# Optimization experiments

Measured on AMD Instinct MI355X. Metric: run time of the kernel, lower is better.

Reference implementation:

```python
import jax, jax.numpy as jnp
import numpy as np

K = 40  # neighbors, self.k = 40 in the module
BN_EPS = 1e-5


def knn(x, k):
    # x: (B, C, N) -> indices of k nearest points (largest negative sq-dist)
    xx = jnp.sum(x * x, axis=1, keepdims=True)            # (B, 1, N)
    inner = -2.0 * jnp.einsum('bcn,bcm->bnm', x, x)       # (B, N, N)
    pd = -xx - inner - jnp.swapaxes(xx, 1, 2)             # (B, N, N) = -||xi-xj||^2
    _, idx = jax.lax.top_k(pd, k)                         # (B, N, k)
    return idx


def graph_cov(x, k):
    # Faithful port of get_graph_dynamic_covariance (dim9=False, idx=None)
    B, C, N = x.shape
    idx = knn(x, k)                                       # (B, N, k)
    xt = jnp.swapaxes(x, 1, 2)                            # (B, N, C)
    feature = xt[jnp.arange(B)[:, None, None], idx]       # gather: (B, N, k, C)
    xc = xt[:, :, None, :]                                # (B, N, 1, C)
    rel = feature - xc                                    # relative positions
    var = jnp.var(rel, axis=2, ddof=1)                    # torch.var is unbiased
    relf = rel * (1.0 - var)[:, :, None, :]
    relf = jnp.concatenate([jnp.broadcast_to(xc, rel.shape), relf], axis=3)
    norm = rel - jnp.mean(rel, axis=0)                    # mean over BATCH dim, as in source
    cov = jnp.einsum('bnkc,bnjc->bnkj', rel, norm)        # (B, N, k, k)
    out = jnp.concatenate([relf, cov], axis=3)            # (B, N, k, 2C+k)
    return jnp.transpose(out, (0, 3, 1, 2))               # (B, 2C+k, N, k)


def bn(x, g, b):
    # train-mode BatchNorm (batch statistics, biased variance), eps=1e-5
    axes = (0,) + tuple(range(2, x.ndim))
    m = jnp.mean(x, axis=axes, keepdims=True)
    v = jnp.var(x, axis=axes, keepdims=True)
    shp = (1, -1) + (1,) * (x.ndim - 2)
    return g.reshape(shp) * (x - m) * jax.lax.rsqrt(v + BN_EPS) + b.reshape(shp)


def blk(x, W, g, b):
    # Conv(1x1, no bias) + BN + LeakyReLU(0.2)
    return jax.nn.leaky_relu(bn(jnp.einsum('oi,bi...->bo...', W, x), g, b), 0.2)


def forward(x, l, W3, W4, W5, W6, W7, W8, W9, W10, W11, W12,
            g3, b3, g4, b4, g5, b5, g6, b6, g7, b7, g8, b8, g9, b9,
            g10, b10, g11, b11):
    B, _, N = x.shape
    rc = blk(blk(graph_cov(x, K), W3, g3, b3), W4, g4, b4)       # (B,64,N,K)
    rc_ = jnp.max(rc, axis=-1)                                    # (B,64,N)
    drc = blk(blk(graph_cov(rc_, K), W5, g5, b5), W6, g6, b6)
    drc_ = jnp.max(drc, axis=-1)                                  # (B,64,N)
    allf = jnp.concatenate([rc_, drc_], axis=1)                   # (B,128,N)
    h = jnp.max(blk(allf, W7, g7, b7), axis=-1, keepdims=True)    # (B,1024,1)
    lv = blk(l.reshape(B, -1, 1), W8, g8, b8)                     # (B,64,1)
    h = jnp.concatenate([h, lv], axis=1)                          # (B,1088,1)
    h = jnp.broadcast_to(h, (B, h.shape[1], N))
    h = jnp.concatenate([h, rc_, drc_], axis=1)                   # (B,1216,N)
    h = blk(h, W9, g9, b9)
    h = blk(h, W10, g10, b10)                                     # dropout is eval-mode identity
    h = blk(h, W11, g11, b11)
    return jnp.einsum('oi,bin->bon', W12, h)                      # (B,50,N)


def setup_inputs():
    key = jax.random.key(0)
    ks = jax.random.split(key, 12)
    B, N = 4, 2048
    d = {}
    d['x'] = jax.random.normal(ks[0], (B, 3, N), jnp.float32)
    lab = jax.random.randint(ks[1], (B,), 0, 16)
    d['l'] = jax.nn.one_hot(lab, 16, dtype=jnp.float32)
    wdims = {'W3': (64, 46), 'W4': (64, 64), 'W5': (64, 168), 'W6': (64, 64),
             'W7': (1024, 128), 'W8': (64, 16), 'W9': (512, 1216),
             'W10': (256, 512), 'W11': (128, 256), 'W12': (50, 128)}
    for i, (name, shp) in enumerate(wdims.items()):
        d[name] = jax.random.normal(ks[2 + i], shp, jnp.float32) / np.float32(np.sqrt(shp[1]))
    for name, c in [('g3', 64), ('g4', 64), ('g5', 64), ('g6', 64), ('g7', 1024),
                    ('g8', 64), ('g9', 512), ('g10', 256), ('g11', 128)]:
        d[name] = jnp.ones((c,), jnp.float32)
        d['b' + name[1:]] = jnp.zeros((c,), jnp.float32)
    return d


def reference(x, l, W3, W4, W5, W6, W7, W8, W9, W10, W11, W12,
              g3, b3, g4, b4, g5, b5, g6, b6, g7, b7, g8, b8, g9, b9,
              g10, b10, g11, b11):
    return forward(x, l, W3, W4, W5, W6, W7, W8, W9, W10, W11, W12,
                   g3, b3, g4, b4, g5, b5, g6, b6, g7, b7, g8, b8, g9, b9,
                   g10, b10, g11, b11)
```

## Files before the change

### kernel.cpp

```cpp
#include <hip/hip_runtime.h>
#include <math.h>

#define NB 4
#define NP 2048
#define KNN 40
#define BEPS 1e-5f
#define NSLOT 64
#define CMCH 16

typedef unsigned long long u64;

static __device__ __forceinline__ float leaky(float x) { return x >= 0.f ? x : 0.2f * x; }

static __device__ __forceinline__ u64 keyOf(float v, int m) {
  unsigned u = __float_as_uint(v);
  u ^= (u >> 31) ? 0xFFFFFFFFu : 0x80000000u;
  return ((u64)u << 32) | (unsigned)(NP - 1 - m);
}
static __device__ __forceinline__ u64 umax64(u64 a, u64 b) { return a > b ? a : b; }

__global__ __launch_bounds__(256) void canary_kernel(float* __restrict__ out, int n, float val) {
  int i = blockIdx.x*256 + threadIdx.x;
  if (i < n) out[i] = val;
}

__global__ __launch_bounds__(256) void knn3_kernel(const float* __restrict__ x, int* __restrict__ idx) {
  int b = blockIdx.y, n = blockIdx.x, tid = threadIdx.x;
  __shared__ float pd[NP];
  __shared__ u64 red[256];
  __shared__ u64 red2[32];
  __shared__ int sh_w;
  float xn0 = x[(b*3+0)*NP+n], xn1 = x[(b*3+1)*NP+n], xn2 = x[(b*3+2)*NP+n];
  float xxn = __fadd_rn(__fadd_rn(__fmul_rn(xn0,xn0), __fmul_rn(xn1,xn1)), __fmul_rn(xn2,xn2));
  for (int m = tid; m < NP; m += 256) {
    float m0 = x[(b*3+0)*NP+m], m1 = x[(b*3+1)*NP+m], m2 = x[(b*3+2)*NP+m];
    float xxm = __fadd_rn(__fadd_rn(__fmul_rn(m0,m0), __fmul_rn(m1,m1)), __fmul_rn(m2,m2));
    float dot = __fmaf_rn(xn2, m2, __fmaf_rn(xn1, m1, __fmul_rn(xn0, m0)));
    float inner = __fmul_rn(-2.f, dot);
    pd[m] = __fsub_rn(__fsub_rn(-xxm, inner), xxn);
  }
  __syncthreads();
  u64 myBest = 0;
  #pragma unroll
  for (int j = 0; j < 8; ++j) myBest = umax64(myBest, keyOf(pd[tid + j*256], tid + j*256));
  for (int kk = 0; kk < KNN; ++kk) {
    red[tid] = myBest;
    __syncthreads();
    if (tid < 32) {
      u64 h = red[tid];
      #pragma unroll
      for (int j = 1; j < 8; ++j) h = umax64(h, red[tid + j*32]);
      red2[tid] = h;
    }
    __syncthreads();
    if (tid == 0) {
      u64 h = red2[0];
      #pragma unroll
      for (int j = 1; j < 32; ++j) h = umax64(h, red2[j]);
      int w = NP - 1 - (int)(h & 0xFFFFFFFFu);
      idx[(b*NP+n)*KNN + kk] = w;
      pd[w] = -INFINITY;
      sh_w = w;
    }
    __syncthreads();
    if ((sh_w & 255) == tid) {
      u64 nb = 0;
      #pragma unroll
      for (int j = 0; j < 8; ++j) nb = umax64(nb, keyOf(pd[tid + j*256], tid + j*256));
      myBest = nb;
    }
  }
}

__global__ __launch_bounds__(256) void xx64_kernel(const float* __restrict__ rc, float* __restrict__ xx) {
  int i = blockIdx.x*256 + threadIdx.x;
  if (i >= NB*NP) return;
  const float* p = &rc[(size_t)i*64];
  float s = __fmul_rn(p[0], p[0]);
  #pragma unroll
  for (int c = 1; c < 64; ++c) s = __fadd_rn(s, __fmul_rn(p[c], p[c]));
  xx[i] = s;
}

__global__ __launch_bounds__(256) void knn64_kernel(const float* __restrict__ rc, const float* __restrict__ xx,
                                                    int* __restrict__ idx) {
  int b = blockIdx.y, n0 = blockIdx.x*2, tid = threadIdx.x;
  __shared__ float pd[2][NP];
  __shared__ float xn[2][64];
  __shared__ u64 red[256];
  __shared__ u64 red2[32];
  __shared__ int sh_w;
  if (tid < 128) xn[tid >> 6][tid & 63] = rc[((size_t)b*NP + n0 + (tid >> 6))*64 + (tid & 63)];
  __syncthreads();
  float xxn0 = xx[b*NP + n0], xxn1 = xx[b*NP + n0 + 1];
  for (int m = tid; m < NP; m += 256) {
    const float* xm = &rc[((size_t)b*NP + m)*64];
    float v0 = xm[0];
    float d0 = __fmul_rn(xn[0][0], v0);
    float d1 = __fmul_rn(xn[1][0], v0);
    #pragma unroll
    for (int c = 1; c < 64; ++c) {
      float v = xm[c];
      d0 = __fmaf_rn(xn[0][c], v, d0);
      d1 = __fmaf_rn(xn[1][c], v, d1);
    }
    float xxm = xx[b*NP + m];
    pd[0][m] = __fsub_rn(__fsub_rn(-xxm, __fmul_rn(-2.f, d0)), xxn0);
    pd[1][m] = __fsub_rn(__fsub_rn(-xxm, __fmul_rn(-2.f, d1)), xxn1);
  }
  __syncthreads();
  for (int q = 0; q < 2; ++q) {
    u64 myBest = 0;
    #pragma unroll
    for (int j = 0; j < 8; ++j) myBest = umax64(myBest, keyOf(pd[q][tid + j*256], tid + j*256));
    for (int kk = 0; kk < KNN; ++kk) {
      red[tid] = myBest;
      __syncthreads();
      if (tid < 32) {
        u64 h = red[tid];
        #pragma unroll
        for (int j = 1; j < 8; ++j) h = umax64(h, red[tid + j*32]);
        red2[tid] = h;
      }
      __syncthreads();
      if (tid == 0) {
        u64 h = red2[0];
        #pragma unroll
        for (int j = 1; j < 32; ++j) h = umax64(h, red2[j]);
        int w = NP - 1 - (int)(h & 0xFFFFFFFFu);
        idx[((size_t)b*NP + n0 + q)*KNN + kk] = w;
        pd[q][w] = -INFINITY;
        sh_w = w;
      }
      __syncthreads();
      if ((sh_w & 255) == tid) {
        u64 nb = 0;
        #pragma unroll
        for (int j = 0; j < 8; ++j) nb = umax64(nb, keyOf(pd[q][tid + j*256], tid + j*256));
        myBest = nb;
      }
    }
    __syncthreads();
  }
}


__global__ __launch_bounds__(256) void s1a_kernel(
    const float* __restrict__ x, const int* __restrict__ idx1, const float* __restrict__ W3,
    double* __restrict__ stslots, float* __restrict__ y)
{
  int b = blockIdx.y, n = blockIdx.x, tid = threadIdx.x;
  __shared__ int sidx[4][KNN];
  __shared__ float rs[KNN][4];
  __shared__ float ns[KNN][4];
  __shared__ float scale[3];
  __shared__ __align__(16) float feat[KNN*48];
  __shared__ float w3s[64*48];
  __shared__ double sred[4][64];

  for (int i = tid; i < 4*KNN; i += 256) sidx[i/KNN][i%KNN] = idx1[((i/KNN)*NP + n)*KNN + (i%KNN)];
  for (int i = tid; i < 64*48; i += 256) { int o = i/48, ci = i%48; w3s[i] = (ci < 46) ? W3[o*46+ci] : 0.f; }
  __syncthreads();
  for (int i = tid; i < KNN*3; i += 256) {
    int k = i/3, c = i%3;
    float ctr = x[(b*3+c)*NP + n];
    float r = x[(b*3+c)*NP + sidx[b][k]] - ctr;
    float s = 0.f;
    for (int b2 = 0; b2 < 4; ++b2) s += x[(b2*3+c)*NP + sidx[b2][k]] - x[(b2*3+c)*NP + n];
    rs[k][c] = r; ns[k][c] = r - 0.25f*s;
  }
  __syncthreads();
  if (tid < 3) {
    float s = 0.f; for (int k = 0; k < KNN; ++k) s += rs[k][tid];
    float m = s/(float)KNN; float v = 0.f;
    for (int k = 0; k < KNN; ++k) { float d = rs[k][tid]-m; v += d*d; }
    scale[tid] = 1.f - v/(float)(KNN-1);
  }
  __syncthreads();
  for (int i = tid; i < KNN*48; i += 256) {
    int k = i/48, ci = i%48; float v;
    if (ci < 3) v = x[(b*3+ci)*NP+n];
    else if (ci < 6) v = rs[k][ci-3]*scale[ci-3];
    else if (ci < 46) { int j = ci-6; v = rs[k][0]*ns[j][0] + rs[k][1]*ns[j][1] + rs[k][2]*ns[j][2]; }
    else v = 0.f;
    feat[i] = v;
  }
  __syncthreads();

  int o = tid & 63, kg = tid >> 6;
  float acc[10];
  #pragma unroll
  for (int t = 0; t < 10; ++t) acc[t] = 0.f;
  for (int ci4 = 0; ci4 < 12; ++ci4) {
    float w0 = w3s[o*48+ci4*4+0], w1 = w3s[o*48+ci4*4+1], w2 = w3s[o*48+ci4*4+2], w3c = w3s[o*48+ci4*4+3];
    #pragma unroll
    for (int t = 0; t < 10; ++t) {
      float4 f4 = *(const float4*)&feat[(kg*10+t)*48 + ci4*4];
      acc[t] += f4.x*w0 + f4.y*w1 + f4.z*w2 + f4.w*w3c;
    }
  }
  size_t bn40 = (size_t)(b*NP+n)*KNN;
  #pragma unroll
  for (int t = 0; t < 10; ++t) y[(bn40 + kg*10+t)*64 + o] = acc[t];
  double s = 0.0, s2 = 0.0;
  #pragma unroll
  for (int t = 0; t < 10; ++t) { double a = acc[t]; s += a; s2 += a*a; }
  int slot = (blockIdx.y*NP + blockIdx.x) & (NSLOT-1);
  sred[kg][o] = s; __syncthreads();
  if (kg == 0) atomicAdd(&stslots[slot*128 + o], sred[0][o]+sred[1][o]+sred[2][o]+sred[3][o]);
  __syncthreads();
  sred[kg][o] = s2; __syncthreads();
  if (kg == 0) atomicAdd(&stslots[slot*128 + 64 + o], sred[0][o]+sred[1][o]+sred[2][o]+sred[3][o]);
}

__global__ __launch_bounds__(256) void s2a_kernel(
    const float* __restrict__ rc, const int* __restrict__ idx2, const float* __restrict__ W5,
    double* __restrict__ stslots, float* __restrict__ y)
{
  int b = blockIdx.y, n = blockIdx.x, tid = threadIdx.x;
  __shared__ int sidx[4][KNN];
  __shared__ float rsT[64*41];
  __shared__ float nsT[64*41];
  __shared__ float scale[64];
  __shared__ __align__(16) float feat[KNN*168];
  __shared__ double sred[4][64];

  for (int i = tid; i < 4*KNN; i += 256) sidx[i/KNN][i%KNN] = idx2[((i/KNN)*NP + n)*KNN + (i%KNN)];
  __syncthreads();
  for (int i = tid; i < KNN*64; i += 256) {
    int k = i >> 6, c = i & 63;
    float ctr = rc[((size_t)(b*NP+n))*64 + c];
    float r = rc[((size_t)(b*NP) + sidx[b][k])*64 + c] - ctr;
    float s = 0.f;
    for (int b2 = 0; b2 < 4; ++b2)
      s += rc[((size_t)(b2*NP) + sidx[b2][k])*64 + c] - rc[((size_t)(b2*NP+n))*64 + c];
    rsT[c*41+k] = r; nsT[c*41+k] = r - 0.25f*s;
  }
  __syncthreads();
  if (tid < 64) {
    int c = tid;
    float s = 0.f; for (int k = 0; k < KNN; ++k) s += rsT[c*41+k];
    float m = s/(float)KNN; float v = 0.f;
    for (int k = 0; k < KNN; ++k) { float d = rsT[c*41+k]-m; v += d*d; }
    scale[c] = 1.f - v/(float)(KNN-1);
  }
  __syncthreads();
  for (int i = tid; i < KNN*128; i += 256) {
    int k = i >> 7, ci = i & 127;
    float v;
    if (ci < 64) v = rc[((size_t)(b*NP+n))*64 + ci];
    else v = rsT[(ci-64)*41 + k]*scale[ci-64];
    feat[k*168 + ci] = v;
  }
  for (int p = tid; p < KNN*KNN; p += 256) {
    int k = p/KNN, j = p%KNN;
    float acc = __fmul_rn(rsT[k], nsT[j]);
    #pragma unroll 8
    for (int c = 1; c < 64; ++c) acc = __fmaf_rn(rsT[c*41+k], nsT[c*41+j], acc);
    feat[k*168 + 128 + j] = acc;
  }
  __syncthreads();

  int o = tid & 63, kg = tid >> 6;
  float acc[10];
  #pragma unroll
  for (int t = 0; t < 10; ++t) acc[t] = 0.f;
  for (int ci4 = 0; ci4 < 42; ++ci4) {
    float4 wv = *(const float4*)&W5[(size_t)o*168 + ci4*4];
    #pragma unroll
    for (int t = 0; t < 10; ++t) {
      float4 f4 = *(const float4*)&feat[(kg*10+t)*168 + ci4*4];
      acc[t] += f4.x*wv.x + f4.y*wv.y + f4.z*wv.z + f4.w*wv.w;
    }
  }
  size_t bn40 = (size_t)(b*NP+n)*KNN;
  #pragma unroll
  for (int t = 0; t < 10; ++t) y[(bn40 + kg*10+t)*64 + o] = acc[t];
  double s = 0.0, s2 = 0.0;
  #pragma unroll
  for (int t = 0; t < 10; ++t) { double a = acc[t]; s += a; s2 += a*a; }
  int slot = (blockIdx.y*NP + blockIdx.x) & (NSLOT-1);
  sred[kg][o] = s; __syncthreads();
  if (kg == 0) atomicAdd(&stslots[slot*128 + o], sred[0][o]+sred[1][o]+sred[2][o]+sred[3][o]);
  __syncthreads();
  sred[kg][o] = s2; __syncthreads();
  if (kg == 0) atomicAdd(&stslots[slot*128 + 64 + o], sred[0][o]+sred[1][o]+sred[2][o]+sred[3][o]);
}

__global__ __launch_bounds__(256) void mid_kernel(
    float* __restrict__ y, const float* __restrict__ W,
    const double* __restrict__ stp, const float* __restrict__ gv, const float* __restrict__ bv,
    double* __restrict__ stslots)
{
  int b = blockIdx.y, n = blockIdx.x, tid = threadIdx.x;
  __shared__ float m_s[64], sc_s[64], bo_s[64];
  __shared__ __align__(16) float ytile[KNN*68];
  __shared__ double sred[4][64];
  const double INV_M1 = 1.0/327680.0;

  if (tid < 64) {
    double md = stp[tid]*INV_M1;
    double vd = stp[64+tid]*INV_M1 - md*md;
    m_s[tid] = (float)md;
    sc_s[tid] = gv[tid]/sqrtf((float)vd + BEPS);
    bo_s[tid] = bv[tid];
  }
  __syncthreads();
  size_t bn40 = (size_t)(b*NP+n)*KNN;
  for (int i = tid; i < KNN*64; i += 256) {
    int k = i >> 6, c = i & 63;
    float v = y[(bn40 + k)*64 + c];
    ytile[k*68+c] = leaky(sc_s[c]*(v - m_s[c]) + bo_s[c]);
  }
  __syncthreads();
  int o = tid & 63, kg = tid >> 6;
  float acc2[10];
  #pragma unroll
  for (int t = 0; t < 10; ++t) acc2[t] = 0.f;
  for (int c4 = 0; c4 < 16; ++c4) {
    float4 wv = *(const float4*)&W[(size_t)o*64 + c4*4];
    #pragma unroll
    for (int t = 0; t < 10; ++t) {
      float4 y4 = *(const float4*)&ytile[(kg*10+t)*68 + c4*4];
      acc2[t] += y4.x*wv.x + y4.y*wv.y + y4.z*wv.z + y4.w*wv.w;
    }
  }
  #pragma unroll
  for (int t = 0; t < 10; ++t) y[(bn40 + kg*10+t)*64 + o] = acc2[t];
  double s = 0.0, s2 = 0.0;
  #pragma unroll
  for (int t = 0; t < 10; ++t) { double a = acc2[t]; s += a; s2 += a*a; }
  int slot = (blockIdx.y*NP + blockIdx.x) & (NSLOT-1);
  sred[kg][o] = s; __syncthreads();
  if (kg == 0) atomicAdd(&stslots[slot*128 + o], sred[0][o]+sred[1][o]+sred[2][o]+sred[3][o]);
  __syncthreads();
  sred[kg][o] = s2; __syncthreads();
  if (kg == 0) atomicAdd(&stslots[slot*128 + 64 + o], sred[0][o]+sred[1][o]+sred[2][o]+sred[3][o]);
}

__global__ __launch_bounds__(256) void maxk_bn_kernel(
    const float* __restrict__ y, const double* __restrict__ stp,
    const float* __restrict__ gv, const float* __restrict__ bv, float* __restrict__ out)
{
  int i = blockIdx.x*256 + threadIdx.x;
  if (i >= NB*NP*64) return;
  int o = i & 63; int bn = i >> 6;
  const double INV_M1 = 1.0/327680.0;
  double md = stp[o]*INV_M1;
  double vd = stp[64+o]*INV_M1 - md*md;
  float m = (float)md;
  float sc = gv[o]/sqrtf((float)vd + BEPS);
  float bo = bv[o];
  float mx = -INFINITY;
  size_t base = (size_t)bn*KNN;
  for (int k = 0; k < KNN; ++k) {
    float v = y[(base + k)*64 + o];
    mx = fmaxf(mx, leaky(sc*(v-m) + bo));
  }
  out[(size_t)bn*64 + o] = mx;
}

__global__ __launch_bounds__(128) void redstats_kernel(const double* __restrict__ slots, double* __restrict__ st) {
  int c = threadIdx.x;
  double s = 0.0;
  for (int i = 0; i < NSLOT; ++i) s += slots[i*128 + c];
  st[c] = s;
}

__global__ __launch_bounds__(256) void allf_kernel(const float* __restrict__ rc, const float* __restrict__ drc,
                                                   float* __restrict__ out) {
  int i = blockIdx.x*256 + threadIdx.x;
  if (i >= NB*NP*128) return;
  int c = i & 127; int bn = i >> 7;
  out[i] = (c < 64) ? rc[(size_t)bn*64 + c] : drc[(size_t)bn*64 + (c-64)];
}

#define GBM 64
#define GBN 64
#define GBK 16
__global__ __launch_bounds__(256) void gemm_kernel(const float* __restrict__ A, const float* __restrict__ W,
                                                   float* __restrict__ C, int M, int No, int Kd,
                                                   int wstride, int woff, const float* __restrict__ bias) {
  __shared__ __align__(16) float As[GBK][GBM+8];
  __shared__ __align__(16) float Ws[GBK][GBN+8];
  int bm = blockIdx.y * GBM, bn = blockIdx.x * GBN;
  int tid = threadIdx.x;
  int tx = tid % 16, ty = tid / 16;
  float acc[4][4] = {{0.f}};
  for (int k0 = 0; k0 < Kd; k0 += GBK) {
    for (int i = tid; i < GBM*GBK; i += 256) {
      int r = i / GBK, c = i % GBK;
      int gm = bm + r, gk = k0 + c;
      As[c][r] = (gk < Kd && gm < M) ? A[(size_t)gm*Kd + gk] : 0.f;
      int gn = bn + r;
      Ws[c][r] = (gk < Kd && gn < No) ? W[(size_t)gn*wstride + woff + gk] : 0.f;
    }
    __syncthreads();
    #pragma unroll
    for (int kk = 0; kk < GBK; ++kk) {
      float4 a4 = *(const float4*)&As[kk][ty*4];
      float4 w4 = *(const float4*)&Ws[kk][tx*4];
      float av[4] = {a4.x, a4.y, a4.z, a4.w};
      float wv[4] = {w4.x, w4.y, w4.z, w4.w};
      #pragma unroll
      for (int i2 = 0; i2 < 4; ++i2)
        #pragma unroll
        for (int j2 = 0; j2 < 4; ++j2)
          acc[i2][j2] += av[i2]*wv[j2];
    }
    __syncthreads();
  }
  for (int i2 = 0; i2 < 4; ++i2) {
    int gm = bm + ty*4 + i2;
    if (gm >= M) continue;
    for (int j2 = 0; j2 < 4; ++j2) {
      int gn = bn + tx*4 + j2;
      if (gn < No) {
        float v = acc[i2][j2];
        if (bias) v += bias[(gm >> 11)*No + gn];
        C[(size_t)gm*No + gn] = v;
      }
    }
  }
}

__global__ __launch_bounds__(256) void colstats_kernel(const float* __restrict__ A, long M, int C,
                                                       int rowsPerBlock, double* __restrict__ st) {
  long r0 = (long)blockIdx.x * rowsPerBlock;
  long r1 = r0 + rowsPerBlock; if (r1 > M) r1 = M;
  int tid = threadIdx.x;
  if (C >= 256) {
    for (int c0 = 0; c0 < C; c0 += 256) {
      int c = c0 + tid;
      double s = 0.0, s2 = 0.0;
      for (long r = r0; r < r1; ++r) { double v = A[r*(long)C + c]; s += v; s2 += v*v; }
      atomicAdd(&st[c], s); atomicAdd(&st[C+c], s2);
    }
  } else {
    int c = tid % C; int grp = tid / C; int G = 256 / C;
    double s = 0.0, s2 = 0.0;
    for (long r = r0 + grp; r < r1; r += G) { double v = A[r*(long)C + c]; s += v; s2 += v*v; }
    __shared__ double sh[512];
    sh[tid] = s; sh[256+tid] = s2; __syncthreads();
    for (int g = G/2; g > 0; g >>= 1) {
      if (grp < g) { sh[tid] += sh[tid + g*C]; sh[256+tid] += sh[256+tid + g*C]; }
      __syncthreads();
    }
    if (grp == 0) { atomicAdd(&st[c], sh[tid]); atomicAdd(&st[C+c], sh[256+tid]); }
  }
}

__global__ __launch_bounds__(256) void bnapply_kernel(float* __restrict__ A, const double* __restrict__ st,
                                                      const float* __restrict__ g, const float* __restrict__ bb,
                                                      double invM, int cmask, size_t total) {
  size_t i = (size_t)blockIdx.x*256 + threadIdx.x;
  if (i >= total) return;
  int c = (int)(i & cmask);
  int C = cmask + 1;
  double md = st[c]*invM;
  double vd = st[C+c]*invM - md*md;
  float m = (float)md;
  float sc = g[c]/sqrtf((float)vd + BEPS);
  float y = sc*(A[i]-m) + bb[c];
  A[i] = leaky(y);
}

__global__ __launch_bounds__(256) void colmax_part_kernel(const float* __restrict__ A, int C,
                                                          float* __restrict__ pmax) {
  int i = blockIdx.x*256 + threadIdx.x;
  if (i >= NB*CMCH*C) return;
  int c = i % C; int t = i / C; int ch = t % CMCH; int b = t / CMCH;
  int n0 = ch * (NP/CMCH);
  float mx = -INFINITY;
  for (int n = n0; n < n0 + NP/CMCH; ++n)
    mx = fmaxf(mx, A[((size_t)(b*NP+n))*C + c]);
  pmax[(size_t)(b*CMCH+ch)*C + c] = mx;
}
__global__ __launch_bounds__(256) void colmax_fin_kernel(const float* __restrict__ pmax, int C,
                                                         float* __restrict__ out) {
  int i = blockIdx.x*256 + threadIdx.x;
  if (i >= NB*C) return;
  int b = i / C, c = i % C;
  float mx = -INFINITY;
  for (int ch = 0; ch < CMCH; ++ch) mx = fmaxf(mx, pmax[(size_t)(b*CMCH+ch)*C + c]);
  out[i] = mx;
}

__global__ __launch_bounds__(256) void lv_kernel(const float* __restrict__ l, const float* __restrict__ W8,
                                                 const float* __restrict__ g8, const float* __restrict__ b8,
                                                 float* __restrict__ lv) {
  __shared__ float raw[4][64];
  int tid = threadIdx.x;
  {
    int b = tid / 64, o = tid % 64;
    float s = 0.f;
    for (int i = 0; i < 16; ++i) s += W8[o*16+i]*l[b*16+i];
    raw[b][o] = s;
  }
  __syncthreads();
  if (tid < 64) {
    int o = tid;
    float m = (raw[0][o]+raw[1][o]+raw[2][o]+raw[3][o])*0.25f;
    float v = 0.f;
    for (int b = 0; b < 4; ++b) { float d = raw[b][o]-m; v += d*d; }
    v *= 0.25f;
    float sc = g8[o]/sqrtf(v + BEPS);
    for (int b = 0; b < 4; ++b) {
      float y = sc*(raw[b][o]-m) + b8[o];
      lv[b*64+o] = leaky(y);
    }
  }
}

__global__ __launch_bounds__(256) void bias9_kernel(const float* __restrict__ hmax, const float* __restrict__ lv,
                                                    const float* __restrict__ W9, float* __restrict__ bias9) {
  int i = blockIdx.x*256 + threadIdx.x;
  if (i >= 4*512) return;
  int b = i >> 9, o = i & 511;
  const float* wr = &W9[(size_t)o*1216];
  float s = 0.f;
  for (int c = 0; c < 1024; ++c) s += hmax[b*1024+c]*wr[c];
  for (int c = 0; c < 64; ++c) s += lv[b*64+c]*wr[1024+c];
  bias9[i] = s;
}

__global__ __launch_bounds__(256) void out_kernel(const float* __restrict__ h5, float* __restrict__ out) {
  int i = blockIdx.x*256 + threadIdx.x;
  if (i >= NB*50*NP) return;
  int n = i % NP; int t = i / NP; int o = t % 50; int b = t / 50;
  out[i] = h5[((size_t)(b*NP+n))*50 + o];
}

extern "C" void kernel_launch(void* const* d_in, const int* in_sizes, int n_in,
                              void* d_out, int out_size, void* d_ws, size_t ws_size,
                              hipStream_t stream) {
  const float* x   = (const float*)d_in[0];
  const float* l   = (const float*)d_in[1];
  const float* W3  = (const float*)d_in[2];
  const float* W4  = (const float*)d_in[3];
  const float* W5  = (const float*)d_in[4];
  const float* W6  = (const float*)d_in[5];
  const float* W7  = (const float*)d_in[6];
  const float* W8  = (const float*)d_in[7];
  const float* W9  = (const float*)d_in[8];
  const float* W10 = (const float*)d_in[9];
  const float* W11 = (const float*)d_in[10];
  const float* W12 = (const float*)d_in[11];
  const float* g3 = (const float*)d_in[12], *b3 = (const float*)d_in[13];
  const float* g4 = (const float*)d_in[14], *b4 = (const float*)d_in[15];
  const float* g5 = (const float*)d_in[16], *b5 = (const float*)d_in[17];
  const float* g6 = (const float*)d_in[18], *b6 = (const float*)d_in[19];
  const float* g7 = (const float*)d_in[20], *b7 = (const float*)d_in[21];
  const float* g8 = (const float*)d_in[22], *b8 = (const float*)d_in[23];
  const float* g9 = (const float*)d_in[24], *b9 = (const float*)d_in[25];
  const float* g10 = (const float*)d_in[26], *b10 = (const float*)d_in[27];
  const float* g11 = (const float*)d_in[28], *b11 = (const float*)d_in[29];
  (void)in_sizes; (void)n_in;

  constexpr size_t OFF_IDX1 = 0;
  constexpr size_t OFF_IDX2 = OFF_IDX1 + (size_t)NB*NP*KNN*4;
  constexpr size_t OFF_RC   = OFF_IDX2 + (size_t)NB*NP*KNN*4;
  constexpr size_t OFF_DRC  = OFF_RC   + (size_t)NB*NP*64*4;
  constexpr size_t OFF_XX   = OFF_DRC  + (size_t)NB*NP*64*4;
  constexpr size_t OFF_SLOT = OFF_XX   + (size_t)NB*NP*4;
  constexpr size_t OFF_ST3  = OFF_SLOT + (size_t)NSLOT*128*8;
  constexpr size_t OFF_ST4  = OFF_ST3 + 128*8;
  constexpr size_t OFF_ST5  = OFF_ST4 + 128*8;
  constexpr size_t OFF_ST6  = OFF_ST5 + 128*8;
  constexpr size_t OFF_STH  = OFF_ST6 + 128*8;
  constexpr size_t OFF_HMAX = OFF_STH + 2*1024*8;
  constexpr size_t OFF_LV   = OFF_HMAX + 4*1024*4;
  constexpr size_t OFF_B9   = OFF_LV + 4096;
  constexpr size_t OFF_PMAX = OFF_B9 + 4*512*4;
  constexpr size_t OFF_ALLF = OFF_PMAX + (size_t)NB*CMCH*1024*4;
  constexpr size_t OFF_H1   = OFF_ALLF + (size_t)NB*NP*128*4;
  constexpr size_t SZ_H1    = (size_t)NB*NP*1024*4;
  constexpr size_t OFF_END  = OFF_H1 + SZ_H1;
  constexpr size_t OFF_H2 = OFF_H1;
  constexpr size_t OFF_H3 = OFF_H2 + (size_t)NB*NP*512*4;
  constexpr size_t OFF_H4 = OFF_H3 + (size_t)NB*NP*256*4;
  constexpr size_t OFF_H5 = OFF_H4 + (size_t)NB*NP*128*4;
  static_assert(OFF_H5 + (size_t)NB*NP*50*4 <= OFF_END, "h alias overflow");
  constexpr size_t OFF_Y   = OFF_END;
  constexpr size_t SZ_Y    = (size_t)NB*NP*KNN*64*4;
  constexpr size_t OFF_FAST_END = OFF_Y + SZ_Y;

  if (ws_size < OFF_END) {
    canary_kernel<<<(out_size + 255)/256, 256, 0, stream>>>((float*)d_out, out_size, (float)(ws_size >> 20));
    return;
  }
  const bool FAST = (ws_size >= OFF_FAST_END);

  char* ws = (char*)d_ws;
  int*    idx1  = (int*)(ws + OFF_IDX1);
  int*    idx2  = (int*)(ws + OFF_IDX2);
  float*  rc    = (float*)(ws + OFF_RC);
  float*  drc   = (float*)(ws + OFF_DRC);
  float*  xx2   = (float*)(ws + OFF_XX);
  double* slots = (double*)(ws + OFF_SLOT);
  double* st3s  = (double*)(ws + OFF_ST3);
  double* st4s  = (double*)(ws + OFF_ST4);
  double* st5s  = (double*)(ws + OFF_ST5);
  double* st6s  = (double*)(ws + OFF_ST6);
  double* sth   = (double*)(ws + OFF_STH);
  float*  hmaxb = (float*)(ws + OFF_HMAX);
  float*  lvb   = (float*)(ws + OFF_LV);
  float*  bias9 = (float*)(ws + OFF_B9);
  float*  pmaxb = (float*)(ws + OFF_PMAX);
  float*  allf  = (float*)(ws + OFF_ALLF);
  float*  h1    = (float*)(ws + OFF_H1);
  float*  h2    = (float*)(ws + OFF_H2);
  float*  h3    = (float*)(ws + OFF_H3);
  float*  h4    = (float*)(ws + OFF_H4);
  float*  h5    = (float*)(ws + OFF_H5);
  float*  ybuf  = (float*)(ws + OFF_Y);

  dim3 gridNP(NP, NB);
  dim3 gridKNN2(NP/2, NB);
  const size_t slotBytes = (size_t)NSLOT*128*8;
  const double INV_M2 = 1.0/8192.0;

  knn3_kernel<<<gridNP, 256, 0, stream>>>(x, idx1);
  hipMemsetAsync(slots, 0, slotBytes, stream);
  s1a_kernel<<<gridNP, 256, 0, stream>>>(x, idx1, W3, slots, FAST ? ybuf : h1);
  redstats_kernel<<<1, 128, 0, stream>>>(slots, st3s);
  hipMemsetAsync(slots, 0, slotBytes, stream);
  mid_kernel<<<gridNP, 256, 0, stream>>>(FAST ? ybuf : h1, W4, st3s, g3, b3, slots);
  redstats_kernel<<<1, 128, 0, stream>>>(slots, st4s);
  maxk_bn_kernel<<<(NB*NP*64 + 255)/256, 256, 0, stream>>>(FAST ? ybuf : h1, st4s, g4, b4, rc);

  xx64_kernel<<<(NB*NP + 255)/256, 256, 0, stream>>>(rc, xx2);
  knn64_kernel<<<gridKNN2, 256, 0, stream>>>(rc, xx2, idx2);
  hipMemsetAsync(slots, 0, slotBytes, stream);
  s2a_kernel<<<gridNP, 256, 0, stream>>>(rc, idx2, W5, slots, FAST ? ybuf : h1);
  redstats_kernel<<<1, 128, 0, stream>>>(slots, st5s);
  hipMemsetAsync(slots, 0, slotBytes, stream);
  mid_kernel<<<gridNP, 256, 0, stream>>>(FAST ? ybuf : h1, W6, st5s, g5, b5, slots);
  redstats_kernel<<<1, 128, 0, stream>>>(slots, st6s);
  maxk_bn_kernel<<<(NB*NP*64 + 255)/256, 256, 0, stream>>>(FAST ? ybuf : h1, st6s, g6, b6, drc);

  allf_kernel<<<(NB*NP*128 + 255)/256, 256, 0, stream>>>(rc, drc, allf);
  gemm_kernel<<<dim3(1024/GBN, 8192/GBM), 256, 0, stream>>>(allf, W7, h1, 8192, 1024, 128, 128, 0, nullptr);
  hipMemsetAsync(sth, 0, 2*1024*8, stream);
  colstats_kernel<<<128, 256, 0, stream>>>(h1, 8192, 1024, 64, sth);
  bnapply_kernel<<<(unsigned)(((size_t)8192*1024 + 255)/256), 256, 0, stream>>>(h1, sth, g7, b7, INV_M2, 1023, (size_t)8192*1024);
  colmax_part_kernel<<<(NB*CMCH*1024 + 255)/256, 256, 0, stream>>>(h1, 1024, pmaxb);
  colmax_fin_kernel<<<(NB*1024 + 255)/256, 256, 0, stream>>>(pmaxb, 1024, hmaxb);
  lv_kernel<<<1, 256, 0, stream>>>(l, W8, g8, b8, lvb);
  bias9_kernel<<<8, 256, 0, stream>>>(hmaxb, lvb, W9, bias9);

  gemm_kernel<<<dim3(512/GBN, 8192/GBM), 256, 0, stream>>>(allf, W9, h2, 8192, 512, 128, 1216, 1088, bias9);
  hipMemsetAsync(sth, 0, 2*512*8, stream);
  colstats_kernel<<<128, 256, 0, stream>>>(h2, 8192, 512, 64, sth);
  bnapply_kernel<<<(unsigned)(((size_t)8192*512 + 255)/256), 256, 0, stream>>>(h2, sth, g9, b9, INV_M2, 511, (size_t)8192*512);

  gemm_kernel<<<dim3(256/GBN, 8192/GBM), 256, 0, stream>>>(h2, W10, h3, 8192, 256, 512, 512, 0, nullptr);
  hipMemsetAsync(sth, 0, 2*256*8, stream);
  colstats_kernel<<<128, 256, 0, stream>>>(h3, 8192, 256, 64, sth);
  bnapply_kernel<<<(unsigned)(((size_t)8192*256 + 255)/256), 256, 0, stream>>>(h3, sth, g10, b10, INV_M2, 255, (size_t)8192*256);

  gemm_kernel<<<dim3(128/GBN, 8192/GBM), 256, 0, stream>>>(h3, W11, h4, 8192, 128, 256, 256, 0, nullptr);
  hipMemsetAsync(sth, 0, 2*128*8, stream);
  colstats_kernel<<<128, 256, 0, stream>>>(h4, 8192, 128, 64, sth);
  bnapply_kernel<<<(unsigned)(((size_t)8192*128 + 255)/256), 256, 0, stream>>>(h4, sth, g11, b11, INV_M2, 127, (size_t)8192*128);

  gemm_kernel<<<dim3(1, 8192/GBM), 256, 0, stream>>>(h4, W12, h5, 8192, 50, 128, 128, 0, nullptr);
  out_kernel<<<(NB*50*NP + 255)/256, 256, 0, stream>>>(h5, (float*)d_out);
}
```

Before: 1.784 ms.

## Select top-40 for two query points concurrently using half-block reductions

Introduces a shared select40_dual routine in which each 128-thread half of the block runs the iterative argmax selection for a different query point, so the two queries share one set of barriers. Previously the two queries were processed one after the other, and knn3 handled a single query per block. knn3 now computes two queries per block and launches half as many blocks. Each thread now scans 16 candidates instead of 8 when refreshing its local best, and shared memory per block grows.

```diff
diff --git a/kernel.cpp b/kernel.cpp
--- a/kernel.cpp
+++ b/kernel.cpp
@@ -19,57 +19,75 @@
 }
 static __device__ __forceinline__ u64 umax64(u64 a, u64 b) { return a > b ? a : b; }
 
+static __device__ __forceinline__ void select40_dual(float (*pd)[NP], int* __restrict__ out0,
+                                                     int* __restrict__ out1, int tid,
+                                                     u64* red, u64* red2, int* sh_w) {
+  int h = tid >> 7, t = tid & 127;
+  int* outp = h ? out1 : out0;
+  u64 myBest = 0;
+  #pragma unroll
+  for (int j = 0; j < 16; ++j) myBest = umax64(myBest, keyOf(pd[h][t + j*128], t + j*128));
+  for (int kk = 0; kk < KNN; ++kk) {
+    red[tid] = myBest;
+    __syncthreads();
+    if (t < 16) {
+      u64 v = red[h*128 + t];
+      #pragma unroll
+      for (int j = 1; j < 8; ++j) v = umax64(v, red[h*128 + t + j*16]);
+      red2[h*16 + t] = v;
+    }
+    __syncthreads();
+    if (t == 0) {
+      u64 v = red2[h*16];
+      #pragma unroll
+      for (int j = 1; j < 16; ++j) v = umax64(v, red2[h*16 + j]);
+      int w = NP - 1 - (int)(v & 0xFFFFFFFFu);
+      outp[kk] = w;
+      pd[h][w] = -INFINITY;
+      sh_w[h] = w;
+    }
+    __syncthreads();
+    if ((sh_w[h] & 127) == t) {
+      u64 nb = 0;
+      #pragma unroll
+      for (int j = 0; j < 16; ++j) nb = umax64(nb, keyOf(pd[h][t + j*128], t + j*128));
+      myBest = nb;
+    }
+  }
+}
+
 __global__ __launch_bounds__(256) void canary_kernel(float* __restrict__ out, int n, float val) {
   int i = blockIdx.x*256 + threadIdx.x;
   if (i < n) out[i] = val;
 }
 
 __global__ __launch_bounds__(256) void knn3_kernel(const float* __restrict__ x, int* __restrict__ idx) {
-  int b = blockIdx.y, n = blockIdx.x, tid = threadIdx.x;
-  __shared__ float pd[NP];
+  int b = blockIdx.y, n0 = blockIdx.x*2, tid = threadIdx.x;
+  __shared__ float pd[2][NP];
+  __shared__ float xq[2][3];
+  __shared__ float xxq[2];
   __shared__ u64 red[256];
   __shared__ u64 red2[32];
-  __shared__ int sh_w;
-  float xn0 = x[(b*3+0)*NP+n], xn1 = x[(b*3+1)*NP+n], xn2 = x[(b*3+2)*NP+n];
-  float xxn = __fadd_rn(__fadd_rn(__fmul_rn(xn0,xn0), __fmul_rn(xn1,xn1)), __fmul_rn(xn2,xn2));
+  __shared__ int sh_w[2];
+  if (tid < 2) {
+    int n = n0 + tid;
+    float a0 = x[(b*3+0)*NP+n], a1 = x[(b*3+1)*NP+n], a2 = x[(b*3+2)*NP+n];
+    xq[tid][0] = a0; xq[tid][1] = a1; xq[tid][2] = a2;
+    xxq[tid] = __fadd_rn(__fadd_rn(__fmul_rn(a0,a0), __fmul_rn(a1,a1)), __fmul_rn(a2,a2));
+  }
+  __syncthreads();
   for (int m = tid; m < NP; m += 256) {
     float m0 = x[(b*3+0)*NP+m], m1 = x[(b*3+1)*NP+m], m2 = x[(b*3+2)*NP+m];
     float xxm = __fadd_rn(__fadd_rn(__fmul_rn(m0,m0), __fmul_rn(m1,m1)), __fmul_rn(m2,m2));
-    float dot = __fmaf_rn(xn2, m2, __fmaf_rn(xn1, m1, __fmul_rn(xn0, m0)));
-    float inner = __fmul_rn(-2.f, dot);
-    pd[m] = __fsub_rn(__fsub_rn(-xxm, inner), xxn);
-  }
-  __syncthreads();
-  u64 myBest = 0;
-  #pragma unroll
-  for (int j = 0; j < 8; ++j) myBest = umax64(myBest, keyOf(pd[tid + j*256], tid + j*256));
-  for (int kk = 0; kk < KNN; ++kk) {
-    red[tid] = myBest;
-    __syncthreads();
-    if (tid < 32) {
-      u64 h = red[tid];
-      #pragma unroll
-      for (int j = 1; j < 8; ++j) h = umax64(h, red[tid + j*32]);
-      red2[tid] = h;
-    }
-    __syncthreads();
-    if (tid == 0) {
-      u64 h = red2[0];
-      #pragma unroll
-      for (int j = 1; j < 32; ++j) h = umax64(h, red2[j]);
-      int w = NP - 1 - (int)(h & 0xFFFFFFFFu);
-      idx[(b*NP+n)*KNN + kk] = w;
-      pd[w] = -INFINITY;
-      sh_w = w;
-    }
-    __syncthreads();
-    if ((sh_w & 255) == tid) {
-      u64 nb = 0;
-      #pragma unroll
-      for (int j = 0; j < 8; ++j) nb = umax64(nb, keyOf(pd[tid + j*256], tid + j*256));
-      myBest = nb;
-    }
-  }
+    #pragma unroll
+    for (int q = 0; q < 2; ++q) {
+      float dot = __fmaf_rn(xq[q][2], m2, __fmaf_rn(xq[q][1], m1, __fmul_rn(xq[q][0], m0)));
+      float inner = __fmul_rn(-2.f, dot);
+      pd[q][m] = __fsub_rn(__fsub_rn(-xxm, inner), xxq[q]);
+    }
+  }
+  __syncthreads();
+  select40_dual(pd, &idx[((size_t)b*NP + n0)*KNN], &idx[((size_t)b*NP + n0 + 1)*KNN], tid, red, red2, sh_w);
 }
 
 __global__ __launch_bounds__(256) void xx64_kernel(const float* __restrict__ rc, float* __restrict__ xx) {
@@ -89,7 +107,7 @@
   __shared__ float xn[2][64];
   __shared__ u64 red[256];
   __shared__ u64 red2[32];
-  __shared__ int sh_w;
+  __shared__ int sh_w[2];
   if (tid < 128) xn[tid >> 6][tid & 63] = rc[((size_t)b*NP + n0 + (tid >> 6))*64 + (tid & 63)];
   __syncthreads();
   float xxn0 = xx[b*NP + n0], xxn1 = xx[b*NP + n0 + 1];
@@ -109,39 +127,7 @@
     pd[1][m] = __fsub_rn(__fsub_rn(-xxm, __fmul_rn(-2.f, d1)), xxn1);
   }
   __syncthreads();
-  for (int q = 0; q < 2; ++q) {
-    u64 myBest = 0;
-    #pragma unroll
-    for (int j = 0; j < 8; ++j) myBest = umax64(myBest, keyOf(pd[q][tid + j*256], tid + j*256));
-    for (int kk = 0; kk < KNN; ++kk) {
-      red[tid] = myBest;
-      __syncthreads();
-      if (tid < 32) {
-        u64 h = red[tid];
-        #pragma unroll
-        for (int j = 1; j < 8; ++j) h = umax64(h, red[tid + j*32]);
-        red2[tid] = h;
-      }
-      __syncthreads();
-      if (tid == 0) {
-        u64 h = red2[0];
-        #pragma unroll
-        for (int j = 1; j < 32; ++j) h = umax64(h, red2[j]);
-        int w = NP - 1 - (int)(h & 0xFFFFFFFFu);
-        idx[((size_t)b*NP + n0 + q)*KNN + kk] = w;
-        pd[q][w] = -INFINITY;
-        sh_w = w;
-      }
-      __syncthreads();
-      if ((sh_w & 255) == tid) {
-        u64 nb = 0;
-        #pragma unroll
-        for (int j = 0; j < 8; ++j) nb = umax64(nb, keyOf(pd[q][tid + j*256], tid + j*256));
-        myBest = nb;
-      }
-    }
-    __syncthreads();
-  }
+  select40_dual(pd, &idx[((size_t)b*NP + n0)*KNN], &idx[((size_t)b*NP + n0 + 1)*KNN], tid, red, red2, sh_w);
 }
 
 
@@ -620,7 +606,7 @@
   const size_t slotBytes = (size_t)NSLOT*128*8;
   const double INV_M2 = 1.0/8192.0;
 
-  knn3_kernel<<<gridNP, 256, 0, stream>>>(x, idx1);
+  knn3_kernel<<<gridKNN2, 256, 0, stream>>>(x, idx1);
   hipMemsetAsync(slots, 0, slotBytes, stream);
   s1a_kernel<<<gridNP, 256, 0, stream>>>(x, idx1, W3, slots, FAST ? ybuf : h1);
   redstats_kernel<<<1, 128, 0, stream>>>(slots, st3s);
```

After: 1.523 ms. 14.6% less time.
